# Kernel optimization log

Measured on AMD Instinct MI355X. Metric: run time of the kernel, lower is better.

## Reference

```python
import jax, jax.numpy as jnp
import numpy as np

N = 50000        # nodes
E = 800000       # edges (avg degree 16)
HID = 96         # hidden_channels
HEADS = 4        # heads passed to SRGATConv
D = HID // HEADS # per-head dim
R = 38           # num_relations
NEG_SLOPE = 0.2  # LeakyReLU slope for attention logits


def setup_inputs() -> dict:
    key = jax.random.key(0)
    ks = jax.random.split(key, 9)
    x = jax.random.normal(ks[0], (N, HID), jnp.float32)
    edge_index = jax.random.randint(ks[1], (2, E), 0, N, dtype=jnp.int32)
    edge_type = jax.random.randint(ks[2], (E,), 0, R, dtype=jnp.int32)
    s = 1.0 / np.sqrt(HID)
    W = jax.random.normal(ks[3], (HID, HID), jnp.float32) * s          # node projection
    rel_emb = jax.random.normal(ks[4], (R, HID), jnp.float32) * s      # relation embeddings
    att_src = jax.random.normal(ks[5], (HEADS, D), jnp.float32) * 0.1  # attention vectors
    att_dst = jax.random.normal(ks[6], (HEADS, D), jnp.float32) * 0.1
    att_rel = jax.random.normal(ks[7], (HEADS, D), jnp.float32) * 0.1
    bias = jnp.zeros((HID,), jnp.float32)
    return {"x": x, "edge_index": edge_index, "edge_type": edge_type,
            "W": W, "rel_emb": rel_emb, "att_src": att_src,
            "att_dst": att_dst, "att_rel": att_rel, "bias": bias}


def reference(x, edge_index, edge_type, W, rel_emb, att_src, att_dst, att_rel, bias):
    # SRGATConv: relation-aware multi-head graph attention, then GELU wrapper.
    n = x.shape[0]
    src, dst = edge_index[0], edge_index[1]
    h = (x @ W).reshape(n, HEADS, D)                    # [N,H,D]
    r = rel_emb[edge_type].reshape(-1, HEADS, D)        # [E,H,D] gathered relation feats
    h_src = h[src]                                      # [E,H,D] irregular gather
    h_dst = h[dst]
    # attention logits per edge/head
    logits = ((h_src * att_src).sum(-1)
              + (h_dst * att_dst).sum(-1)
              + (r * att_rel).sum(-1))                  # [E,H]
    logits = jax.nn.leaky_relu(logits, NEG_SLOPE)
    # segment softmax over incoming edges of each destination node
    lmax = jax.ops.segment_max(logits, dst, num_segments=n)   # [N,H]
    e = jnp.exp(logits - lmax[dst])
    denom = jax.ops.segment_sum(e, dst, num_segments=n)       # [N,H]
    alpha = e / denom[dst]                                    # [E,H]
    # weighted message scatter
    msg = alpha[:, :, None] * (h_src + r)                     # [E,H,D]
    out = jax.ops.segment_sum(msg, dst, num_segments=n).reshape(n, HID) + bias
    out = jax.nn.gelu(out)
    return out, alpha
```

## Files before the change

### kernel.cpp

```cpp
#include <hip/hip_runtime.h>
#include <hip/hip_fp16.h>
#include <math.h>

#define HIDC 96
#define HEADS 4
#define RMAX 40
#define BINSZ 128
#define BINCAP 2560
#define TILE 2048
#define SRCB 18
#define SRCM ((1 << SRCB) - 1)
#define ETB 6

typedef unsigned u32x2 __attribute__((ext_vector_type(2)));
typedef int i32x4 __attribute__((ext_vector_type(4)));

__device__ __forceinline__ __half2 u2h2(unsigned u) {
    return *reinterpret_cast<__half2*>(&u);
}
__device__ __forceinline__ unsigned h22u(__half2 h) {
    return *reinterpret_cast<unsigned*>(&h);
}

__global__ __launch_bounds__(192) void gemm96(const float* __restrict__ x,
                                              const float* __restrict__ W,
                                              __half* __restrict__ h16,
                                              int* __restrict__ bincnt,
                                              int n, int nbins) {
    for (int i = blockIdx.x * 192 + threadIdx.x; i < nbins; i += gridDim.x * 192)
        bincnt[i] = 0;

    __shared__ float Ws[HIDC * HIDC];
    __shared__ float xs[32 * HIDC];
    for (int i = threadIdx.x; i < HIDC * HIDC / 4; i += 192)
        reinterpret_cast<float4*>(Ws)[i] = reinterpret_cast<const float4*>(W)[i];
    int c4 = threadIdx.x % 24;
    int r0 = (threadIdx.x / 24) * 4;
    const float4* xs4 = reinterpret_cast<const float4*>(xs);
    const float4* Ws4 = reinterpret_cast<const float4*>(Ws);
    uint2* h8 = reinterpret_cast<uint2*>(h16);
    int numTiles = (n + 31) >> 5;
    for (int tile = blockIdx.x; tile < numTiles; tile += gridDim.x) {
        int row0 = tile << 5;
        int rows = min(32, n - row0);
        __syncthreads();
        for (int i = threadIdx.x; i < rows * 24; i += 192)
            reinterpret_cast<float4*>(xs)[i] =
                reinterpret_cast<const float4*>(x + (size_t)row0 * HIDC)[i];
        __syncthreads();
        float4 acc[4];
#pragma unroll
        for (int i = 0; i < 4; ++i) acc[i] = make_float4(0.f, 0.f, 0.f, 0.f);
#pragma unroll 4
        for (int k4 = 0; k4 < 24; ++k4) {
            float4 xv[4], wv[4];
#pragma unroll
            for (int i = 0; i < 4; ++i) xv[i] = xs4[(r0 + i) * 24 + k4];
#pragma unroll
            for (int j = 0; j < 4; ++j) wv[j] = Ws4[(k4 * 4 + j) * 24 + c4];
#pragma unroll
            for (int i = 0; i < 4; ++i) {
                const float xi[4] = {xv[i].x, xv[i].y, xv[i].z, xv[i].w};
#pragma unroll
                for (int j = 0; j < 4; ++j) {
                    acc[i].x = fmaf(xi[j], wv[j].x, acc[i].x);
                    acc[i].y = fmaf(xi[j], wv[j].y, acc[i].y);
                    acc[i].z = fmaf(xi[j], wv[j].z, acc[i].z);
                    acc[i].w = fmaf(xi[j], wv[j].w, acc[i].w);
                }
            }
        }
#pragma unroll
        for (int i = 0; i < 4; ++i)
            if (r0 + i < rows) {
                __half2 lo = __floats2half2_rn(acc[i].x, acc[i].y);
                __half2 hi = __floats2half2_rn(acc[i].z, acc[i].w);
                uint2 pk;
                pk.x = h22u(lo);
                pk.y = h22u(hi);
                h8[(size_t)(row0 + r0 + i) * 24 + c4] = pk;
            }
    }
}

__global__ __launch_bounds__(256) void node_dots(
    const __half* __restrict__ h16,
    const float* __restrict__ att_src, const float* __restrict__ att_dst,
    const float* __restrict__ rel, const float* __restrict__ att_rel,
    float4* __restrict__ ps, float* __restrict__ pdi,
    float4* __restrict__ pr, int n, int R_) {
    if (blockIdx.x == gridDim.x - 1) {
        int t = threadIdx.x;
        if (t < R_) {
            const float4* rp = reinterpret_cast<const float4*>(rel + (size_t)t * HIDC);
            const float4* ar = reinterpret_cast<const float4*>(att_rel);
            float acc[HEADS] = {0, 0, 0, 0};
#pragma unroll
            for (int c = 0; c < 24; ++c) {
                float4 v = rp[c], a = ar[c];
                acc[c / 6] += v.x * a.x + v.y * a.y + v.z * a.z + v.w * a.w;
            }
            pr[t] = make_float4(acc[0], acc[1], acc[2], acc[3]);
        }
        return;
    }
    int i = blockIdx.x * blockDim.x + threadIdx.x;
    if (i >= n) return;
    const uint2* hp = reinterpret_cast<const uint2*>(h16 + (size_t)i * HIDC);
    const float4* as = reinterpret_cast<const float4*>(att_src);
    const float4* ad = reinterpret_cast<const float4*>(att_dst);
    float accs[HEADS] = {0, 0, 0, 0}, accd[HEADS] = {0, 0, 0, 0};
#pragma unroll
    for (int c = 0; c < 24; ++c) {
        uint2 hv = hp[c];
        float2 f0 = __half22float2(u2h2(hv.x));
        float2 f1 = __half22float2(u2h2(hv.y));
        float4 a = as[c], d = ad[c];
        int hh = c / 6;
        accs[hh] += f0.x * a.x + f0.y * a.y + f1.x * a.z + f1.y * a.w;
        accd[hh] += f0.x * d.x + f0.y * d.y + f1.x * d.z + f1.y * d.w;
    }
    ps[i] = make_float4(accs[0], accs[1], accs[2], accs[3]);
    *reinterpret_cast<float4*>(pdi + (size_t)i * 8) =
        make_float4(accd[0], accd[1], accd[2], accd[3]);
}

__device__ __forceinline__ float4 ev4(float4 a, float4 b, float4 c) {
    float l0 = a.x + b.x + c.x, l1 = a.y + b.y + c.y;
    float l2 = a.z + b.z + c.z, l3 = a.w + b.w + c.w;
    l0 = l0 >= 0.f ? l0 : 0.2f * l0;
    l1 = l1 >= 0.f ? l1 : 0.2f * l1;
    l2 = l2 >= 0.f ? l2 : 0.2f * l2;
    l3 = l3 >= 0.f ? l3 : 0.2f * l3;
    return make_float4(__expf(l0), __expf(l1), __expf(l2), __expf(l3));
}

__device__ __forceinline__ float gelu_f(float v) {
    float u = 0.7978845608028654f * (v + 0.044715f * v * v * v);
    u = fminf(fmaxf(u, -15.f), 15.f);
    float t = __expf(2.f * u);
    return 0.5f * v * (1.f + (t - 1.f) / (t + 1.f));
}

__global__ __launch_bounds__(256) void bin_edges(
    const int* __restrict__ src, const int* __restrict__ dst,
    const int* __restrict__ et,
    int* __restrict__ bincnt, int* __restrict__ binwords,
    int E_, int nbins) {
    __shared__ int hist[512];
    __shared__ int base[512];
    int e0 = blockIdx.x * TILE;
    for (int i = threadIdx.x; i < nbins; i += 256) hist[i] = 0;
    __syncthreads();
    int mybin[8], myrank[8], myword[8];
#pragma unroll
    for (int u = 0; u < 8; ++u) {
        int e = e0 + u * 256 + threadIdx.x;
        mybin[u] = -1;
        if (e < E_) {
            int d = dst[e];
            int b = d >> 7;
            myword[u] = src[e] | (et[e] << SRCB) | ((d & (BINSZ - 1)) << (SRCB + ETB));
            mybin[u] = b;
            myrank[u] = atomicAdd(&hist[b], 1);
        }
    }
    __syncthreads();
    for (int i = threadIdx.x; i < nbins; i += 256)
        base[i] = hist[i] > 0 ? atomicAdd(&bincnt[i], hist[i]) : 0;
    __syncthreads();
#pragma unroll
    for (int u = 0; u < 8; ++u) {
        if (mybin[u] >= 0) {
            int pos = base[mybin[u]] + myrank[u];
            if (pos < BINCAP)
                binwords[(size_t)mybin[u] * BINCAP + pos] = myword[u];
        }
    }
}

__global__ __launch_bounds__(256) void bin_sort(
    const int* __restrict__ bincnt, const int* __restrict__ binwords,
    const float4* __restrict__ ps, const float* __restrict__ pdi,
    const float4* __restrict__ prg,
    int4* __restrict__ csr, int* __restrict__ noff, int* __restrict__ ncnt,
    int n, int R_) {
    __shared__ int cnts[BINSZ];
    __shared__ int scanb[BINSZ];
    __shared__ int nbase[BINSZ];
    __shared__ float4 pdl[BINSZ];
    __shared__ float4 prl[RMAX];
    int bin = blockIdx.x;
    int node0 = bin * BINSZ;
    int total = min(bincnt[bin], BINCAP);

    for (int i = threadIdx.x; i < BINSZ; i += 256) {
        cnts[i] = 0;
        int nd = node0 + i;
        pdl[i] = (nd < n) ? *reinterpret_cast<const float4*>(pdi + (size_t)nd * 8)
                          : make_float4(0.f, 0.f, 0.f, 0.f);
    }
    for (int i = threadIdx.x; i < R_; i += 256) prl[i] = prg[i];
    __syncthreads();

    int w[10], rk[10];
#pragma unroll
    for (int u = 0; u < 10; ++u) {
        int k = u * 256 + threadIdx.x;
        rk[u] = -1;
        if (k < total) {
            w[u] = binwords[(size_t)bin * BINCAP + k];
            int dl = (w[u] >> (SRCB + ETB)) & (BINSZ - 1);
            rk[u] = atomicAdd(&cnts[dl], 1);
        }
    }
    __syncthreads();

    if (threadIdx.x < BINSZ) scanb[threadIdx.x] = (cnts[threadIdx.x] + 3) & ~3;
    __syncthreads();
    for (int s = 1; s < BINSZ; s <<= 1) {
        int v = 0;
        if (threadIdx.x < BINSZ && threadIdx.x >= s) v = scanb[threadIdx.x - s];
        __syncthreads();
        if (threadIdx.x < BINSZ) scanb[threadIdx.x] += v;
        __syncthreads();
    }
    if (threadIdx.x < BINSZ) {
        int cnt = cnts[threadIdx.x];
        int cntP = (cnt + 3) & ~3;
        int nb = scanb[threadIdx.x] - cntP;
        nbase[threadIdx.x] = nb;
        int nd = node0 + threadIdx.x;
        if (nd < n) {
            noff[nd] = bin * BINCAP + nb;
            ncnt[nd] = cnt;
        }
        int4 z = make_int4(0, 0, 0, 0);
        for (int i = cnt; i < cntP; ++i)
            csr[(size_t)bin * BINCAP + nb + i] = z;
    }
    __syncthreads();

#pragma unroll
    for (int u = 0; u < 10; ++u) {
        if (rk[u] >= 0) {
            int s = w[u] & SRCM;
            int t = (w[u] >> SRCB) & ((1 << ETB) - 1);
            int dl = (w[u] >> (SRCB + ETB)) & (BINSZ - 1);
            float4 v = ev4(ps[s], pdl[dl], prl[t]);
            int4 pk;
            pk.x = s * (HIDC * 2);
            pk.y = t * (HIDC * 2);
            pk.z = (int)h22u(__floats2half2_rn(v.x, v.y));
            pk.w = (int)h22u(__floats2half2_rn(v.z, v.w));
            csr[(size_t)bin * BINCAP + nbase[dl] + rk[u]] = pk;
        }
    }
}

#define EDGE(C, HV, RV)                                                        \
    {                                                                          \
        unsigned e32 = __builtin_amdgcn_perm((unsigned)(C)[3], (unsigned)(C)[2], esel); \
        dsum += __half2float(__low2half(u2h2(e32)));                           \
        unsigned s01 = h22u(__hadd2(u2h2((HV)[0]), u2h2((RV)[0])));            \
        unsigned s23 = h22u(__hadd2(u2h2((HV)[1]), u2h2((RV)[1])));            \
        asm("v_fma_mix_f32 %0, %1, %2, %0 op_sel:[0,0,0] op_sel_hi:[1,1,0]"    \
            : "+v"(a0) : "v"(s01), "v"(e32));                                  \
        asm("v_fma_mix_f32 %0, %1, %2, %0 op_sel:[1,0,0] op_sel_hi:[1,1,0]"    \
            : "+v"(a1) : "v"(s01), "v"(e32));                                  \
        asm("v_fma_mix_f32 %0, %1, %2, %0 op_sel:[0,0,0] op_sel_hi:[1,1,0]"    \
            : "+v"(a2) : "v"(s23), "v"(e32));                                  \
        asm("v_fma_mix_f32 %0, %1, %2, %0 op_sel:[1,0,0] op_sel_hi:[1,1,0]"    \
            : "+v"(a3) : "v"(s23), "v"(e32));                                  \
    }

#define AGG_STEP(C0, C1, C2, C3, N0, N1, N2, N3)                               \
    {                                                                          \
        asm volatile("s_waitcnt vmcnt(0)" ::: "memory");                       \
        __builtin_amdgcn_sched_barrier(0);                                     \
        u32x2 hv0, hv1, hv2, hv3;                                              \
        asm volatile("global_load_dwordx2 %0, %1, %2" : "=&v"(hv0)             \
                     : "v"((unsigned)(C0)[0] + joff), "s"(h16c) : "memory");   \
        asm volatile("global_load_dwordx2 %0, %1, %2" : "=&v"(hv1)             \
                     : "v"((unsigned)(C1)[0] + joff), "s"(h16c) : "memory");   \
        asm volatile("global_load_dwordx2 %0, %1, %2" : "=&v"(hv2)             \
                     : "v"((unsigned)(C2)[0] + joff), "s"(h16c) : "memory");   \
        asm volatile("global_load_dwordx2 %0, %1, %2" : "=&v"(hv3)             \
                     : "v"((unsigned)(C3)[0] + joff), "s"(h16c) : "memory");   \
        u32x2 rv0 = *(const u32x2*)(relc + (unsigned)(C0)[1] + joff);          \
        u32x2 rv1 = *(const u32x2*)(relc + (unsigned)(C1)[1] + joff);          \
        u32x2 rv2 = *(const u32x2*)(relc + (unsigned)(C2)[1] + joff);          \
        u32x2 rv3 = *(const u32x2*)(relc + (unsigned)(C3)[1] + joff);          \
        asm volatile("global_load_dwordx4 %0, %4, %5\n\t"                      \
                     "global_load_dwordx4 %1, %4, %5 offset:16\n\t"            \
                     "global_load_dwordx4 %2, %4, %5 offset:32\n\t"            \
                     "global_load_dwordx4 %3, %4, %5 offset:48"                \
                     : "=&v"(N0), "=&v"(N1), "=&v"(N2), "=&v"(N3)              \
                     : "v"(soff), "s"(csrc) : "memory");                       \
        soff += 64u;                                                           \
        asm volatile("s_waitcnt vmcnt(4)" ::: "memory");                       \
        __builtin_amdgcn_sched_barrier(0);                                     \
        EDGE(C0, hv0, rv0);                                                    \
        EDGE(C1, hv1, rv1);                                                    \
        EDGE(C2, hv2, rv2);                                                    \
        EDGE(C3, hv3, rv3);                                                    \
    }

__global__ __launch_bounds__(256) void node_agg(
    const __half* __restrict__ h16, const float* __restrict__ rel,
    const int4* __restrict__ csr, const int* __restrict__ noff,
    const int* __restrict__ ncnt,
    float* __restrict__ pdi, const float* __restrict__ bias,
    float* __restrict__ out, int n, int R_) {
    __shared__ uint2 relh[RMAX * HIDC / 4];
    for (int i = threadIdx.x; i < R_ * 24; i += 256) {
        float4 v = reinterpret_cast<const float4*>(rel)[i];
        uint2 pk;
        pk.x = h22u(__floats2half2_rn(v.x, v.y));
        pk.y = h22u(__floats2half2_rn(v.z, v.w));
        relh[i] = pk;
    }
    __syncthreads();

    int lane = threadIdx.x & 31;
    if (lane >= 24) return;
    const int j = lane;
    const int j4 = 4 * j;
    const int hh = j / 6;
    const unsigned joff = (unsigned)(j << 3);
    const float4 bv = *reinterpret_cast<const float4*>(bias + j4);
    const char* h16c = reinterpret_cast<const char*>(h16);
    const char* relc = reinterpret_cast<const char*>(relh);
    const char* csrc = reinterpret_cast<const char*>(csr);
    const unsigned esel = (unsigned)(2 * hh) | ((unsigned)(2 * hh + 1) << 8);

    int hw0 = (blockIdx.x * blockDim.x + threadIdx.x) >> 5;
    int nHW = (gridDim.x * blockDim.x) >> 5;

    for (int hw = hw0; hw < n; hw += nHW) {
        int cnt = ncnt[hw];
        float a0 = 0.f, a1 = 0.f, a2 = 0.f, a3 = 0.f;
        float dsum = 0.f;

        if (cnt > 0) {
            unsigned soff = (unsigned)noff[hw] * 16u;
            int nq = (cnt + 3) >> 2;
            i32x4 pA0, pA1, pA2, pA3, pB0, pB1, pB2, pB3;
            asm volatile("global_load_dwordx4 %0, %4, %5\n\t"
                         "global_load_dwordx4 %1, %4, %5 offset:16\n\t"
                         "global_load_dwordx4 %2, %4, %5 offset:32\n\t"
                         "global_load_dwordx4 %3, %4, %5 offset:48"
                         : "=&v"(pA0), "=&v"(pA1), "=&v"(pA2), "=&v"(pA3)
                         : "v"(soff), "s"(csrc) : "memory");
            soff += 64u;
            int q = 0;
            for (;;) {
                AGG_STEP(pA0, pA1, pA2, pA3, pB0, pB1, pB2, pB3);
                if (++q >= nq) break;
                AGG_STEP(pB0, pB1, pB2, pB3, pA0, pA1, pA2, pA3);
                if (++q >= nq) break;
            }
            asm volatile("s_waitcnt vmcnt(0)" ::: "memory");
            __builtin_amdgcn_sched_barrier(0);
        }
        float inv = dsum > 0.f ? 1.f / dsum : 0.f;
        if ((j % 6) == 0) pdi[(size_t)hw * 8 + 4 + hh] = inv;
        float4 o;
        o.x = gelu_f(a0 * inv + bv.x);
        o.y = gelu_f(a1 * inv + bv.y);
        o.z = gelu_f(a2 * inv + bv.z);
        o.w = gelu_f(a3 * inv + bv.w);
        *reinterpret_cast<float4*>(out + (size_t)hw * HIDC + j4) = o;
    }
}

__global__ void alpha_edge(const int* __restrict__ src, const int* __restrict__ dst,
                           const int* __restrict__ et,
                           const float4* __restrict__ ps, const float* __restrict__ pdi,
                           const float4* __restrict__ pr,
                           float4* __restrict__ alpha, int E_) {
    int e = blockIdx.x * blockDim.x + threadIdx.x;
    if (e >= E_) return;
    int d = dst[e];
    const float4* rec = reinterpret_cast<const float4*>(pdi + (size_t)d * 8);
    float4 b = rec[0];
    float4 iv = rec[1];
    float4 v = ev4(ps[src[e]], b, pr[et[e]]);
    alpha[e] = make_float4(v.x * iv.x, v.y * iv.y, v.z * iv.z, v.w * iv.w);
}

extern "C" void kernel_launch(void* const* d_in, const int* in_sizes, int n_in,
                              void* d_out, int out_size, void* d_ws, size_t ws_size,
                              hipStream_t stream) {
    const float* x       = (const float*)d_in[0];
    const int*   eidx    = (const int*)d_in[1];
    const int*   etype   = (const int*)d_in[2];
    const float* W       = (const float*)d_in[3];
    const float* rel     = (const float*)d_in[4];
    const float* att_src = (const float*)d_in[5];
    const float* att_dst = (const float*)d_in[6];
    const float* att_rel = (const float*)d_in[7];
    const float* bias    = (const float*)d_in[8];

    int N_ = in_sizes[0] / HIDC;
    int E_ = in_sizes[1] / 2;
    int R_ = in_sizes[4] / HIDC;
    const int* src  = eidx;
    const int* dstp = eidx + E_;
    int nbins = (N_ + BINSZ - 1) / BINSZ;

    char* ws = (char*)d_ws;
    __half* h16      = (__half*)ws; ws += (size_t)N_ * HIDC * 2;
    float4* ps       = (float4*)ws; ws += (size_t)N_ * 16;
    float*  pdi      = (float*)ws;  ws += (size_t)N_ * 32;
    float4* pr       = (float4*)ws; ws += 1024;
    int*    bincnt   = (int*)ws;    ws += (size_t)((nbins + 3) & ~3) * 4;
    int*    noff     = (int*)ws;    ws += (size_t)((N_ + 3) & ~3) * 4;
    int*    ncnt     = (int*)ws;    ws += (size_t)((N_ + 3) & ~3) * 4;
    int*    binwords = (int*)ws;    ws += (size_t)nbins * BINCAP * 4;
    int4*   csr      = (int4*)ws;   ws += (size_t)nbins * BINCAP * 16 + 256;

    float*  outv  = (float*)d_out;
    float4* alpha = (float4*)(outv + (size_t)N_ * HIDC);

    gemm96<<<(N_ + 31) / 32, 192, 0, stream>>>(x, W, h16, bincnt, N_, nbins);

    node_dots<<<(N_ + 255) / 256 + 1, 256, 0, stream>>>(
        h16, att_src, att_dst, rel, att_rel, ps, pdi, pr, N_, R_);

    bin_edges<<<(E_ + TILE - 1) / TILE, 256, 0, stream>>>(
        src, dstp, etype, bincnt, binwords, E_, nbins);

    bin_sort<<<nbins, 256, 0, stream>>>(
        bincnt, binwords, ps, pdi, pr, csr, noff, ncnt, N_, R_);

    node_agg<<<2048, 256, 0, stream>>>(
        h16, rel, csr, noff, ncnt, pdi, bias, outv, N_, R_);

    alpha_edge<<<(E_ + 255) / 256, 256, 0, stream>>>(
        src, dstp, etype, ps, pdi, pr, alpha, E_);
}
```

Before: 200.9 us.

## Deepen node_agg software pipeline to prefetch CSR and feature gathers ahead

```diff
diff --git a/kernel.cpp b/kernel.cpp
--- a/kernel.cpp
+++ b/kernel.cpp
@@ -26,9 +26,12 @@
                                               const float* __restrict__ W,
                                               __half* __restrict__ h16,
                                               int* __restrict__ bincnt,
+                                              int4* __restrict__ csrtail,
                                               int n, int nbins) {
     for (int i = blockIdx.x * 192 + threadIdx.x; i < nbins; i += gridDim.x * 192)
         bincnt[i] = 0;
+    if (blockIdx.x == 0 && threadIdx.x < 16)
+        csrtail[threadIdx.x] = make_int4(0, 0, 0, 0);
 
     __shared__ float Ws[HIDC * HIDC];
     __shared__ float xs[32 * HIDC];
@@ -239,6 +242,14 @@
         for (int i = cnt; i < cntP; ++i)
             csr[(size_t)bin * BINCAP + nb + i] = z;
     }
+    {
+        int gt = scanb[BINSZ - 1];
+        if (threadIdx.x < 12) {
+            int p = gt + threadIdx.x;
+            if (p < BINCAP)
+                csr[(size_t)bin * BINCAP + p] = make_int4(0, 0, 0, 0);
+        }
+    }
     __syncthreads();
 
 #pragma unroll
@@ -274,36 +285,40 @@
             : "+v"(a3) : "v"(s23), "v"(e32));                                  \
     }
 
-#define AGG_STEP(C0, C1, C2, C3, N0, N1, N2, N3)                               \
+#define CSR_LOAD(D0, D1, D2, D3)                                               \
+    asm volatile("global_load_dwordx4 %0, %4, %5\n\t"                          \
+                 "global_load_dwordx4 %1, %4, %5 offset:16\n\t"                \
+                 "global_load_dwordx4 %2, %4, %5 offset:32\n\t"                \
+                 "global_load_dwordx4 %3, %4, %5 offset:48"                    \
+                 : "=&v"(D0), "=&v"(D1), "=&v"(D2), "=&v"(D3)                  \
+                 : "v"(soff), "s"(csrc) : "memory");                           \
+    soff += 64u;
+
+#define GATHER(Ha, Hb, Hc_, Hd, G0, G1, G2, G3)                                \
+    asm volatile("global_load_dwordx2 %0, %1, %2" : "=&v"(Ha)                  \
+                 : "v"((unsigned)(G0)[0] + joff), "s"(h16c) : "memory");       \
+    asm volatile("global_load_dwordx2 %0, %1, %2" : "=&v"(Hb)                  \
+                 : "v"((unsigned)(G1)[0] + joff), "s"(h16c) : "memory");       \
+    asm volatile("global_load_dwordx2 %0, %1, %2" : "=&v"(Hc_)                 \
+                 : "v"((unsigned)(G2)[0] + joff), "s"(h16c) : "memory");       \
+    asm volatile("global_load_dwordx2 %0, %1, %2" : "=&v"(Hd)                  \
+                 : "v"((unsigned)(G3)[0] + joff), "s"(h16c) : "memory");
+
+#define STEP(C0, C1, C2, C3, G0, G1, G2, G3, D0, D1, D2, D3,                   \
+             Hc0, Hc1, Hc2, Hc3, Hn0, Hn1, Hn2, Hn3)                           \
     {                                                                          \
-        asm volatile("s_waitcnt vmcnt(0)" ::: "memory");                       \
+        asm volatile("s_waitcnt vmcnt(4)" ::: "memory");                       \
         __builtin_amdgcn_sched_barrier(0);                                     \
-        u32x2 hv0, hv1, hv2, hv3;                                              \
-        asm volatile("global_load_dwordx2 %0, %1, %2" : "=&v"(hv0)             \
-                     : "v"((unsigned)(C0)[0] + joff), "s"(h16c) : "memory");   \
-        asm volatile("global_load_dwordx2 %0, %1, %2" : "=&v"(hv1)             \
-                     : "v"((unsigned)(C1)[0] + joff), "s"(h16c) : "memory");   \
-        asm volatile("global_load_dwordx2 %0, %1, %2" : "=&v"(hv2)             \
-                     : "v"((unsigned)(C2)[0] + joff), "s"(h16c) : "memory");   \
-        asm volatile("global_load_dwordx2 %0, %1, %2" : "=&v"(hv3)             \
-                     : "v"((unsigned)(C3)[0] + joff), "s"(h16c) : "memory");   \
+        GATHER(Hn0, Hn1, Hn2, Hn3, G0, G1, G2, G3);                            \
+        CSR_LOAD(D0, D1, D2, D3);                                              \
         u32x2 rv0 = *(const u32x2*)(relc + (unsigned)(C0)[1] + joff);          \
         u32x2 rv1 = *(const u32x2*)(relc + (unsigned)(C1)[1] + joff);          \
         u32x2 rv2 = *(const u32x2*)(relc + (unsigned)(C2)[1] + joff);          \
         u32x2 rv3 = *(const u32x2*)(relc + (unsigned)(C3)[1] + joff);          \
-        asm volatile("global_load_dwordx4 %0, %4, %5\n\t"                      \
-                     "global_load_dwordx4 %1, %4, %5 offset:16\n\t"            \
-                     "global_load_dwordx4 %2, %4, %5 offset:32\n\t"            \
-                     "global_load_dwordx4 %3, %4, %5 offset:48"                \
-                     : "=&v"(N0), "=&v"(N1), "=&v"(N2), "=&v"(N3)              \
-                     : "v"(soff), "s"(csrc) : "memory");                       \
-        soff += 64u;                                                           \
-        asm volatile("s_waitcnt vmcnt(4)" ::: "memory");                       \
-        __builtin_amdgcn_sched_barrier(0);                                     \
-        EDGE(C0, hv0, rv0);                                                    \
-        EDGE(C1, hv1, rv1);                                                    \
-        EDGE(C2, hv2, rv2);                                                    \
-        EDGE(C3, hv3, rv3);                                                    \
+        EDGE(C0, Hc0, rv0);                                                    \
+        EDGE(C1, Hc1, rv1);                                                    \
+        EDGE(C2, Hc2, rv2);                                                    \
+        EDGE(C3, Hc3, rv3);                                                    \
     }
 
 __global__ __launch_bounds__(256) void node_agg(
@@ -345,19 +360,34 @@
         if (cnt > 0) {
             unsigned soff = (unsigned)noff[hw] * 16u;
             int nq = (cnt + 3) >> 2;
-            i32x4 pA0, pA1, pA2, pA3, pB0, pB1, pB2, pB3;
-            asm volatile("global_load_dwordx4 %0, %4, %5\n\t"
-                         "global_load_dwordx4 %1, %4, %5 offset:16\n\t"
-                         "global_load_dwordx4 %2, %4, %5 offset:32\n\t"
-                         "global_load_dwordx4 %3, %4, %5 offset:48"
-                         : "=&v"(pA0), "=&v"(pA1), "=&v"(pA2), "=&v"(pA3)
-                         : "v"(soff), "s"(csrc) : "memory");
-            soff += 64u;
+            i32x4 P00, P01, P02, P03, P10, P11, P12, P13;
+            i32x4 P20, P21, P22, P23, P30, P31, P32, P33;
+            u32x2 H00, H01, H02, H03, H10, H11, H12, H13;
+
+            CSR_LOAD(P00, P01, P02, P03);
+            CSR_LOAD(P10, P11, P12, P13);
+            asm volatile("s_waitcnt vmcnt(0)" ::: "memory");
+            __builtin_amdgcn_sched_barrier(0);
+            GATHER(H00, H01, H02, H03, P00, P01, P02, P03);
+            CSR_LOAD(P20, P21, P22, P23);
+
             int q = 0;
             for (;;) {
-                AGG_STEP(pA0, pA1, pA2, pA3, pB0, pB1, pB2, pB3);
+                STEP(P00, P01, P02, P03, P10, P11, P12, P13,
+                     P30, P31, P32, P33, H00, H01, H02, H03,
+                     H10, H11, H12, H13);
                 if (++q >= nq) break;
-                AGG_STEP(pB0, pB1, pB2, pB3, pA0, pA1, pA2, pA3);
+                STEP(P10, P11, P12, P13, P20, P21, P22, P23,
+                     P00, P01, P02, P03, H10, H11, H12, H13,
+                     H00, H01, H02, H03);
+                if (++q >= nq) break;
+                STEP(P20, P21, P22, P23, P30, P31, P32, P33,
+                     P10, P11, P12, P13, H00, H01, H02, H03,
+                     H10, H11, H12, H13);
+                if (++q >= nq) break;
+                STEP(P30, P31, P32, P33, P00, P01, P02, P03,
+                     P20, P21, P22, P23, H10, H11, H12, H13,
+                     H00, H01, H02, H03);
                 if (++q >= nq) break;
             }
             asm volatile("s_waitcnt vmcnt(0)" ::: "memory");
@@ -423,7 +453,8 @@
     float*  outv  = (float*)d_out;
     float4* alpha = (float4*)(outv + (size_t)N_ * HIDC);
 
-    gemm96<<<(N_ + 31) / 32, 192, 0, stream>>>(x, W, h16, bincnt, N_, nbins);
+    gemm96<<<(N_ + 31) / 32, 192, 0, stream>>>(
+        x, W, h16, bincnt, csr + (size_t)nbins * BINCAP, N_, nbins);
 
     node_dots<<<(N_ + 255) / 256 + 1, 256, 0, stream>>>(
         h16, att_src, att_dst, rel, att_rel, ps, pdi, pr, N_, R_);
```

Measured after the change: 208.9 us. 4.0% more time.
